# Optimization experiments

Hardware: AMD Instinct MI355X
Metric: run time of the kernel (lower is better)

The kernel has to match this reference:

```python
import jax, jax.numpy as jnp
import numpy as np

LN_EPS = 1e-5
SN_EPS = 1e-12


def _block(x, W, b, g, be):
    # Linear -> LayerNorm -> CELU, fused as one expression chain
    h = x @ W.T + b
    mu = jnp.mean(h, axis=-1, keepdims=True)
    var = jnp.mean(jnp.square(h - mu), axis=-1, keepdims=True)
    h = (h - mu) * jax.lax.rsqrt(var + LN_EPS) * g + be
    return jax.nn.celu(h)


def _spectral_norm_weight(W, u):
    # One power iteration (torch training-mode behavior), u/v detached.
    v = W.T @ u
    v = v / (jnp.linalg.norm(v) + SN_EPS)
    u2 = W @ v
    u2 = u2 / (jnp.linalg.norm(u2) + SN_EPS)
    sigma = u2 @ (W @ v)
    return W / sigma


def setup_inputs() -> dict:
    key = jax.random.key(0)
    ks = jax.random.split(key, 8)
    B, D = 131072, 512
    sizes = [512, 128, 32, 8]
    inp = {"x": jax.random.normal(ks[0], (B, D), dtype=jnp.float32)}
    fan_in = D
    for i, s in enumerate(sizes, start=1):
        scale = 1.0 / np.sqrt(fan_in)
        inp[f"W{i}"] = jax.random.normal(ks[i], (s, fan_in), dtype=jnp.float32) * scale
        inp[f"b{i}"] = jnp.zeros((s,), dtype=jnp.float32)
        inp[f"g{i}"] = jnp.ones((s,), dtype=jnp.float32)
        inp[f"be{i}"] = jnp.zeros((s,), dtype=jnp.float32)
        fan_in = s
    inp["Wh"] = jax.random.normal(ks[5], (1, 8), dtype=jnp.float32) * (1.0 / np.sqrt(8))
    inp["bh"] = jnp.zeros((1,), dtype=jnp.float32)
    inp["u"] = jax.random.normal(ks[6], (1,), dtype=jnp.float32)
    return inp


def reference(x, W1, b1, g1, be1, W2, b2, g2, be2, W3, b3, g3, be3,
              W4, b4, g4, be4, Wh, bh, u):
    h = _block(x, W1, b1, g1, be1)
    h = _block(h, W2, b2, g2, be2)
    h = _block(h, W3, b3, g3, be3)
    h = _block(h, W4, b4, g4, be4)          # hidden_output: [B, 8]
    Wsn = _spectral_norm_weight(Wh, u)
    return h @ Wsn.T + bh                   # [B, 1]
```

## Files before the change

### kernel.cpp

```cpp
#include <hip/hip_runtime.h>


typedef unsigned short u16;
typedef unsigned int   u32;
typedef __bf16  bf16x8 __attribute__((ext_vector_type(8)));
typedef float   f32x16 __attribute__((ext_vector_type(16)));

__device__ __forceinline__ u16 f2bf(float f) {
    u32 x = __builtin_bit_cast(u32, f);
    x += 0x7FFFu + ((x >> 16) & 1u);
    return (u16)(x >> 16);
}
__device__ __forceinline__ float bfval(u16 h) { return __builtin_bit_cast(float, (u32)h << 16); }
__device__ __forceinline__ u32 pack2(float a, float b) { return (u32)f2bf(a) | ((u32)f2bf(b) << 16); }
__device__ __forceinline__ float celu1(float x) { return x > 0.f ? x : __expf(x) - 1.f; }

#define W1F_OFF 0
#define W2F_OFF 262144
#define W3F_OFF 327680
#define W3LF_OFF 331776
#define NGROUPS 41984

__global__ void prep_weights(const float* __restrict__ W1, const float* __restrict__ W2,
                             const float* __restrict__ W3, u16* __restrict__ wsb) {
    const int g = blockIdx.x * 256 + threadIdx.x;
    if (g < 32768) {
        const int l = g & 63, t = (g >> 6) & 15, ksg = g >> 10;
        const int n = t * 32 + (l & 31);
        const int k0 = ksg * 16 + (l >> 5) * 8;
        u16* dst = wsb + W1F_OFF + g * 8;
        const float* src = W1 + n * 512 + k0;
#pragma unroll
        for (int e = 0; e < 8; ++e) dst[e] = f2bf(src[e]);
    } else if (g < 40960) {
        const int h = g - 32768;
        const int l = h & 63, t = (h >> 6) & 3, ksg = h >> 8;
        const int n = t * 32 + (l & 31);
        const int k0 = ksg * 16 + (l >> 5) * 8;
        u16* dst = wsb + W2F_OFF + h * 8;
        const float* src = W2 + n * 512 + k0;
#pragma unroll
        for (int e = 0; e < 8; ++e) dst[e] = f2bf(src[e]);
    } else if (g < 41472) {
        const int h = g - 40960;
        const int l = h & 63, ksg = h >> 6;
        const int n = l & 31;
        const int k0 = ksg * 16 + (l >> 5) * 8;
        u16* dst = wsb + W3F_OFF + h * 8;
        const float* src = W3 + n * 128 + k0;
#pragma unroll
        for (int e = 0; e < 8; ++e) dst[e] = f2bf(src[e]);
    } else {
        const int h = g - 41472;
        const int l = h & 63, ksg = h >> 6;
        const int n = l & 31;
        const int k0 = ksg * 16 + (l >> 5) * 8;
        u16* dst = wsb + W3LF_OFF + h * 8;
        const float* src = W3 + n * 128 + k0;
#pragma unroll
        for (int e = 0; e < 8; ++e) { float w = src[e]; dst[e] = f2bf(w - bfval(f2bf(w))); }
    }
}

#define PW4 0
#define PB4 256
#define PG4 264
#define PBE4 272
#define PWH 280
#define PBH 288
#define PU  289
#define NPAR 290

__global__ __launch_bounds__(512, 4) void fused_mlp(
    const float* __restrict__ x,
    const u16* __restrict__ W1b, const u16* __restrict__ W2b,
    const u16* __restrict__ W3b, const u16* __restrict__ W3Lb,
    const float* __restrict__ b1, const float* __restrict__ g1, const float* __restrict__ be1,
    const float* __restrict__ b2, const float* __restrict__ g2, const float* __restrict__ be2,
    const float* __restrict__ b3, const float* __restrict__ g3, const float* __restrict__ be3,
    const float* __restrict__ W4, const float* __restrict__ b4, const float* __restrict__ g4,
    const float* __restrict__ be4,
    const float* __restrict__ Wh, const float* __restrict__ bh, const float* __restrict__ uvec,
    float* __restrict__ out)
{
    __shared__ __align__(16) u16 sXH[32][520];
    __shared__ __align__(16) float sPS[32][8];
    __shared__ __align__(16) float sPQ[32][8];
    __shared__ __align__(8)  float2 sMR[32];
    __shared__ __align__(16) float sP[NPAR + 2];

    const int tid = threadIdx.x;
    const int wv = tid >> 6;
    const int lane = tid & 63;
    const int ln = lane & 31;
    const int lh = lane >> 5;
    const int row0 = blockIdx.x * 32;

    const float b1a = b1[wv * 64 + ln],  b1c = b1[wv * 64 + 32 + ln];
    const float g1a = g1[wv * 64 + ln],  g1c = g1[wv * 64 + 32 + ln];
    const float e1a = be1[wv * 64 + ln], e1c = be1[wv * 64 + 32 + ln];
    const int Nt2 = wv & 3;
    const float b2v = b2[Nt2 * 32 + ln], g2v = g2[Nt2 * 32 + ln], e2v = be2[Nt2 * 32 + ln];
    const float b3v = b3[ln], g3v = g3[ln], e3v = be3[ln];

    if (tid < NPAR) {
        float v;
        if      (tid < 256) v = W4[tid];
        else if (tid < 264) v = b4[tid - 256];
        else if (tid < 272) v = g4[tid - 264];
        else if (tid < 280) v = be4[tid - 272];
        else if (tid < 288) v = Wh[tid - 280];
        else if (tid == 288) v = bh[0];
        else                v = uvec[0];
        sP[tid] = v;
    }

    {
        const float4* xp = (const float4*)(x) + (long)blockIdx.x * 4096 + tid;
        float4 q[8];
#pragma unroll
        for (int j = 0; j < 8; ++j) q[j] = xp[j * 512];
        const int r0 = tid >> 7;
        const int c4 = (tid & 127) * 4;
#pragma unroll
        for (int j = 0; j < 8; ++j)
            *(uint2*)(&sXH[j * 4 + r0][c4]) =
                make_uint2(pack2(q[j].x, q[j].y), pack2(q[j].z, q[j].w));
    }
    __syncthreads();

    f32x16 acc[2] = {};
    {
        const u16* wq = W1b + (wv * 2) * 512 + lane * 8;
        bf16x8 Bf[4][2];
#pragma unroll
        for (int s = 0; s < 3; ++s) {
            Bf[s][0] = *(const bf16x8*)(wq + s * 8192);
            Bf[s][1] = *(const bf16x8*)(wq + s * 8192 + 512);
        }
#pragma unroll
        for (int ksg = 0; ksg < 32; ++ksg) {
            const int slot = ksg & 3;
            if (ksg + 3 < 32) {
                const int ps = (ksg + 3) & 3;
                const u16* np = wq + (ksg + 3) * 8192;
                Bf[ps][0] = *(const bf16x8*)(np);
                Bf[ps][1] = *(const bf16x8*)(np + 512);
            }
            bf16x8 a0 = *(const bf16x8*)(&sXH[ln][ksg * 16 + lh * 8]);
            acc[0] = __builtin_amdgcn_mfma_f32_32x32x16_bf16(a0, Bf[slot][0], acc[0], 0, 0, 0);
            acc[1] = __builtin_amdgcn_mfma_f32_32x32x16_bf16(a0, Bf[slot][1], acc[1], 0, 0, 0);
        }
    }

#pragma unroll
    for (int rg = 0; rg < 16; ++rg) {
        acc[0][rg] += b1a; acc[1][rg] += b1c;
    }
#pragma unroll
    for (int rg = 0; rg < 16; ++rg) {
        float s = acc[0][rg] + acc[1][rg];
        float q = acc[0][rg] * acc[0][rg] + acc[1][rg] * acc[1][rg];
#pragma unroll
        for (int m = 1; m < 32; m <<= 1) { s += __shfl_xor(s, m, 64); q += __shfl_xor(q, m, 64); }
        if (ln == 0) {
            const int row = (rg & 3) + 8 * (rg >> 2) + 4 * lh;
            sPS[row][wv] = s; sPQ[row][wv] = q;
        }
    }
    __syncthreads();
    if (tid < 32) {
        float s = 0.f, q = 0.f;
#pragma unroll
        for (int j = 0; j < 8; ++j) { s += sPS[tid][j]; q += sPQ[tid][j]; }
        const float mu = s * (1.f / 512.f);
        const float var = q * (1.f / 512.f) - mu * mu;
        sMR[tid] = make_float2(mu, rsqrtf(var + 1e-5f));
    }
    __syncthreads();
#pragma unroll
    for (int rg = 0; rg < 16; ++rg) {
        const int row = (rg & 3) + 8 * (rg >> 2) + 4 * lh;
        const float2 mr = sMR[row];
        const float h0 = (acc[0][rg] - mr.x) * mr.y * g1a + e1a;
        const float h1v = (acc[1][rg] - mr.x) * mr.y * g1c + e1c;
        sXH[row][wv * 64 + ln] = f2bf(celu1(h0));
        sXH[row][wv * 64 + 32 + ln] = f2bf(celu1(h1v));
    }
    __syncthreads();

    float v2[16];
    if (wv < 4) {
        const u16* w2q = W2b + Nt2 * 512 + lane * 8;
        bf16x8 W2f[4];
#pragma unroll
        for (int s = 0; s < 4; ++s) W2f[s] = *(const bf16x8*)(w2q + s * 2048);
        f32x16 a2 = {}, a2b = {};
        const u16* h1p = &sXH[ln][lh * 8];
#pragma unroll
        for (int ksg = 0; ksg < 32; ++ksg) {
            const int slot = ksg & 3;
            bf16x8 af = *(const bf16x8*)(h1p + ksg * 16);
            if (ksg & 1) a2b = __builtin_amdgcn_mfma_f32_32x32x16_bf16(af, W2f[slot], a2b, 0, 0, 0);
            else         a2  = __builtin_amdgcn_mfma_f32_32x32x16_bf16(af, W2f[slot], a2, 0, 0, 0);
            if (ksg + 4 < 32) W2f[slot] = *(const bf16x8*)(w2q + (ksg + 4) * 2048);
        }
#pragma unroll
        for (int rg = 0; rg < 16; ++rg) v2[rg] = a2[rg] + a2b[rg] + b2v;
#pragma unroll
        for (int rg = 0; rg < 16; ++rg) {
            float s = v2[rg], q = v2[rg] * v2[rg];
#pragma unroll
            for (int m = 1; m < 32; m <<= 1) { s += __shfl_xor(s, m, 64); q += __shfl_xor(q, m, 64); }
            if (ln == 0) {
                const int row = (rg & 3) + 8 * (rg >> 2) + 4 * lh;
                sPS[row][Nt2] = s; sPQ[row][Nt2] = q;
            }
        }
    }
    __syncthreads();
    if (tid < 32) {
        float s = sPS[tid][0] + sPS[tid][1] + sPS[tid][2] + sPS[tid][3];
        float q = sPQ[tid][0] + sPQ[tid][1] + sPQ[tid][2] + sPQ[tid][3];
        const float mu = s * (1.f / 128.f);
        const float var = q * (1.f / 128.f) - mu * mu;
        sMR[tid] = make_float2(mu, rsqrtf(var + 1e-5f));
    }
    __syncthreads();
    if (wv < 4) {
        const int col = Nt2 * 32 + ln;
#pragma unroll
        for (int rg = 0; rg < 16; ++rg) {
            const int row = (rg & 3) + 8 * (rg >> 2) + 4 * lh;
            const float2 mr = sMR[row];
            const float hn = (v2[rg] - mr.x) * mr.y * g2v + e2v;
            const float a = celu1(hn);
            const u16 hi = f2bf(a);
            sXH[row][col] = hi;
            sXH[row][128 + col] = f2bf(a - bfval(hi));
        }
    }
    __syncthreads();

    if (wv == 0) {
        f32x16 a3 = {};
        const u16* w3q  = W3b  + lane * 8;
        const u16* w3lq = W3Lb + lane * 8;
        const u16* h2p  = &sXH[ln][lh * 8];
        const u16* h2lp = &sXH[ln][128 + lh * 8];
#pragma unroll
        for (int ks = 0; ks < 8; ++ks) {
            bf16x8 fa_h = *(const bf16x8*)(h2p  + ks * 16);
            bf16x8 fa_l = *(const bf16x8*)(h2lp + ks * 16);
            bf16x8 fb_h = *(const bf16x8*)(w3q  + ks * 512);
            bf16x8 fb_l = *(const bf16x8*)(w3lq + ks * 512);
            a3 = __builtin_amdgcn_mfma_f32_32x32x16_bf16(fa_h, fb_h, a3, 0, 0, 0);
            a3 = __builtin_amdgcn_mfma_f32_32x32x16_bf16(fa_h, fb_l, a3, 0, 0, 0);
            a3 = __builtin_amdgcn_mfma_f32_32x32x16_bf16(fa_l, fb_h, a3, 0, 0, 0);
        }
#pragma unroll
        for (int rg = 0; rg < 16; ++rg) {
            const float v = a3[rg] + b3v;
            float s = v, q = v * v;
#pragma unroll
            for (int m = 1; m < 32; m <<= 1) { s += __shfl_xor(s, m, 64); q += __shfl_xor(q, m, 64); }
            const float mu = s * (1.f / 32.f);
            const float rs = rsqrtf(q * (1.f / 32.f) - mu * mu + 1e-5f);
            const int row = (rg & 3) + 8 * (rg >> 2) + 4 * lh;
            float* s3 = (float*)&sXH[row][0] + 128;
            s3[ln] = celu1((v - mu) * rs * g3v + e3v);
        }
    }
    __syncthreads();

    if (tid < 256) {
        const int r = tid & 31, o = tid >> 5;
        float h[32];
        const float4* hp = (const float4*)((const float*)&sXH[r][0] + 128);
#pragma unroll
        for (int j = 0; j < 8; ++j) {
            float4 tv = hp[j];
            h[j * 4 + 0] = tv.x; h[j * 4 + 1] = tv.y; h[j * 4 + 2] = tv.z; h[j * 4 + 3] = tv.w;
        }
        float a = sP[PB4 + o];
        const float* w4 = &sP[PW4 + o * 32];
#pragma unroll
        for (int k = 0; k < 32; ++k) a += h[k] * w4[k];
        sPS[r][o] = a;
    }
    __syncthreads();

    if (tid < 32) {
        float v[8];
        float s = 0.f, q = 0.f;
#pragma unroll
        for (int o = 0; o < 8; ++o) { v[o] = sPS[tid][o]; s += v[o]; q += v[o] * v[o]; }
        const float mu = s * 0.125f;
        const float var = q * 0.125f - mu * mu;
        const float rs = rsqrtf(var + 1e-5f);

        float wh[8];
        const float u0 = sP[PU];
        float nv = 0.f;
#pragma unroll
        for (int o = 0; o < 8; ++o) { wh[o] = sP[PWH + o]; float tt = wh[o] * u0; nv += tt * tt; }
        nv = sqrtf(nv);
        const float inv = 1.f / (nv + 1e-12f);
        float s2 = 0.f;
#pragma unroll
        for (int o = 0; o < 8; ++o) s2 += wh[o] * (wh[o] * u0 * inv);
        const float u2 = s2 / (fabsf(s2) + 1e-12f);
        const float sigma = u2 * s2;
        const float isg = 1.f / sigma;

        float y = sP[PBH];
#pragma unroll
        for (int o = 0; o < 8; ++o) {
            const float hn = (v[o] - mu) * rs * sP[PG4 + o] + sP[PBE4 + o];
            y += celu1(hn) * wh[o] * isg;
        }
        out[row0 + tid] = y;
    }
}

extern "C" void kernel_launch(void* const* d_in, const int* in_sizes, int n_in,
                              void* d_out, int out_size, void* d_ws, size_t ws_size,
                              hipStream_t stream) {
    const float* x   = (const float*)d_in[0];
    const float* W1  = (const float*)d_in[1];
    const float* b1  = (const float*)d_in[2];
    const float* g1  = (const float*)d_in[3];
    const float* be1 = (const float*)d_in[4];
    const float* W2  = (const float*)d_in[5];
    const float* b2  = (const float*)d_in[6];
    const float* g2  = (const float*)d_in[7];
    const float* be2 = (const float*)d_in[8];
    const float* W3  = (const float*)d_in[9];
    const float* b3  = (const float*)d_in[10];
    const float* g3  = (const float*)d_in[11];
    const float* be3 = (const float*)d_in[12];
    const float* W4  = (const float*)d_in[13];
    const float* b4  = (const float*)d_in[14];
    const float* g4  = (const float*)d_in[15];
    const float* be4 = (const float*)d_in[16];
    const float* Wh  = (const float*)d_in[17];
    const float* bh  = (const float*)d_in[18];
    const float* u   = (const float*)d_in[19];
    float* out = (float*)d_out;
    u16* wsb = (u16*)d_ws;

    prep_weights<<<dim3(NGROUPS / 256), dim3(256), 0, stream>>>(W1, W2, W3, wsb);

    const int rows = in_sizes[0] / 512;
    fused_mlp<<<dim3(rows / 32), dim3(512), 0, stream>>>(
        x, wsb + W1F_OFF, wsb + W2F_OFF, wsb + W3F_OFF, wsb + W3LF_OFF,
        b1, g1, be1, b2, g2, be2, b3, g3, be3,
        W4, b4, g4, be4, Wh, bh, u, out);
}
```

Measured before the change: 595.6 us.

## Halve block to 4 waves with 4 N-tiles each and drop tail barriers

Moves the fused MLP from 512-thread to 256-thread blocks. Each wave now computes four 32-column tiles of layer 1, and all four waves do useful work in layer 2 instead of leaving four idle. The layer-4/head stage is folded into wave 0 using an LDS waitcnt instead of block barriers, and s_setprio is raised around the MFMA loops. f2bf now uses the native bf16 conversion. In exchange, each wave holds more accumulator registers, and the W1 prefetch depth drops from three stages to two, which risks lower occupancy and more load latency exposed in layer 1.

Result: faster. 512.7 us (-13.9%).

```diff
diff --git a/kernel.cpp b/kernel.cpp
--- a/kernel.cpp
+++ b/kernel.cpp
@@ -7,9 +7,7 @@
 typedef float   f32x16 __attribute__((ext_vector_type(16)));
 
 __device__ __forceinline__ u16 f2bf(float f) {
-    u32 x = __builtin_bit_cast(u32, f);
-    x += 0x7FFFu + ((x >> 16) & 1u);
-    return (u16)(x >> 16);
+    return __builtin_bit_cast(u16, (__bf16)f);
 }
 __device__ __forceinline__ float bfval(u16 h) { return __builtin_bit_cast(float, (u32)h << 16); }
 __device__ __forceinline__ u32 pack2(float a, float b) { return (u32)f2bf(a) | ((u32)f2bf(b) << 16); }
@@ -71,7 +69,7 @@
 #define PU  289
 #define NPAR 290
 
-__global__ __launch_bounds__(512, 4) void fused_mlp(
+__global__ __launch_bounds__(256, 4) void fused_mlp(
     const float* __restrict__ x,
     const u16* __restrict__ W1b, const u16* __restrict__ W2b,
     const u16* __restrict__ W3b, const u16* __restrict__ W3Lb,
@@ -84,8 +82,8 @@
     float* __restrict__ out)
 {
     __shared__ __align__(16) u16 sXH[32][520];
-    __shared__ __align__(16) float sPS[32][8];
-    __shared__ __align__(16) float sPQ[32][8];
+    __shared__ __align__(16) float sPS[32][4];
+    __shared__ __align__(16) float sPQ[32][4];
     __shared__ __align__(8)  float2 sMR[32];
     __shared__ __align__(16) float sP[NPAR + 2];
 
@@ -96,71 +94,79 @@
     const int lh = lane >> 5;
     const int row0 = blockIdx.x * 32;
 
-    const float b1a = b1[wv * 64 + ln],  b1c = b1[wv * 64 + 32 + ln];
-    const float g1a = g1[wv * 64 + ln],  g1c = g1[wv * 64 + 32 + ln];
-    const float e1a = be1[wv * 64 + ln], e1c = be1[wv * 64 + 32 + ln];
-    const int Nt2 = wv & 3;
-    const float b2v = b2[Nt2 * 32 + ln], g2v = g2[Nt2 * 32 + ln], e2v = be2[Nt2 * 32 + ln];
+    float b1v[4], g1v[4], e1v[4];
+#pragma unroll
+    for (int nt = 0; nt < 4; ++nt) {
+        b1v[nt] = b1[wv * 128 + nt * 32 + ln];
+        g1v[nt] = g1[wv * 128 + nt * 32 + ln];
+        e1v[nt] = be1[wv * 128 + nt * 32 + ln];
+    }
+    const float b2v = b2[wv * 32 + ln], g2v = g2[wv * 32 + ln], e2v = be2[wv * 32 + ln];
     const float b3v = b3[ln], g3v = g3[ln], e3v = be3[ln];
 
-    if (tid < NPAR) {
+    for (int i = tid; i < NPAR; i += 256) {
         float v;
-        if      (tid < 256) v = W4[tid];
-        else if (tid < 264) v = b4[tid - 256];
-        else if (tid < 272) v = g4[tid - 264];
-        else if (tid < 280) v = be4[tid - 272];
-        else if (tid < 288) v = Wh[tid - 280];
-        else if (tid == 288) v = bh[0];
-        else                v = uvec[0];
-        sP[tid] = v;
+        if      (i < 256) v = W4[i];
+        else if (i < 264) v = b4[i - 256];
+        else if (i < 272) v = g4[i - 264];
+        else if (i < 280) v = be4[i - 272];
+        else if (i < 288) v = Wh[i - 280];
+        else if (i == 288) v = bh[0];
+        else               v = uvec[0];
+        sP[i] = v;
     }
 
     {
         const float4* xp = (const float4*)(x) + (long)blockIdx.x * 4096 + tid;
-        float4 q[8];
-#pragma unroll
-        for (int j = 0; j < 8; ++j) q[j] = xp[j * 512];
+        float4 q[16];
+#pragma unroll
+        for (int j = 0; j < 16; ++j) q[j] = xp[j * 256];
         const int r0 = tid >> 7;
         const int c4 = (tid & 127) * 4;
 #pragma unroll
-        for (int j = 0; j < 8; ++j)
-            *(uint2*)(&sXH[j * 4 + r0][c4]) =
+        for (int j = 0; j < 16; ++j)
+            *(uint2*)(&sXH[j * 2 + r0][c4]) =
                 make_uint2(pack2(q[j].x, q[j].y), pack2(q[j].z, q[j].w));
     }
     __syncthreads();
 
-    f32x16 acc[2] = {};
-    {
-        const u16* wq = W1b + (wv * 2) * 512 + lane * 8;
-        bf16x8 Bf[4][2];
-#pragma unroll
-        for (int s = 0; s < 3; ++s) {
-            Bf[s][0] = *(const bf16x8*)(wq + s * 8192);
-            Bf[s][1] = *(const bf16x8*)(wq + s * 8192 + 512);
-        }
+    f32x16 acc[4] = {};
+    {
+        const u16* wq = W1b + (wv * 4) * 512 + lane * 8;
+        bf16x8 Bf[2][4];
+#pragma unroll
+        for (int s = 0; s < 2; ++s)
+#pragma unroll
+            for (int nt = 0; nt < 4; ++nt)
+                Bf[s][nt] = *(const bf16x8*)(wq + s * 8192 + nt * 512);
+        __builtin_amdgcn_s_setprio(1);
 #pragma unroll
         for (int ksg = 0; ksg < 32; ++ksg) {
-            const int slot = ksg & 3;
-            if (ksg + 3 < 32) {
-                const int ps = (ksg + 3) & 3;
-                const u16* np = wq + (ksg + 3) * 8192;
-                Bf[ps][0] = *(const bf16x8*)(np);
-                Bf[ps][1] = *(const bf16x8*)(np + 512);
-            }
+            const int slot = ksg & 1;
             bf16x8 a0 = *(const bf16x8*)(&sXH[ln][ksg * 16 + lh * 8]);
             acc[0] = __builtin_amdgcn_mfma_f32_32x32x16_bf16(a0, Bf[slot][0], acc[0], 0, 0, 0);
             acc[1] = __builtin_amdgcn_mfma_f32_32x32x16_bf16(a0, Bf[slot][1], acc[1], 0, 0, 0);
-        }
-    }
-
+            acc[2] = __builtin_amdgcn_mfma_f32_32x32x16_bf16(a0, Bf[slot][2], acc[2], 0, 0, 0);
+            acc[3] = __builtin_amdgcn_mfma_f32_32x32x16_bf16(a0, Bf[slot][3], acc[3], 0, 0, 0);
+            if (ksg + 2 < 32) {
+                const u16* np = wq + (ksg + 2) * 8192;
+#pragma unroll
+                for (int nt = 0; nt < 4; ++nt)
+                    Bf[slot][nt] = *(const bf16x8*)(np + nt * 512);
+            }
+        }
+        __builtin_amdgcn_s_setprio(0);
+    }
+
+#pragma unroll
+    for (int nt = 0; nt < 4; ++nt)
+#pragma unroll
+        for (int rg = 0; rg < 16; ++rg) acc[nt][rg] += b1v[nt];
 #pragma unroll
     for (int rg = 0; rg < 16; ++rg) {
-        acc[0][rg] += b1a; acc[1][rg] += b1c;
-    }
-#pragma unroll
-    for (int rg = 0; rg < 16; ++rg) {
-        float s = acc[0][rg] + acc[1][rg];
-        float q = acc[0][rg] * acc[0][rg] + acc[1][rg] * acc[1][rg];
+        float s = acc[0][rg] + acc[1][rg] + acc[2][rg] + acc[3][rg];
+        float q = acc[0][rg] * acc[0][rg] + acc[1][rg] * acc[1][rg]
+                + acc[2][rg] * acc[2][rg] + acc[3][rg] * acc[3][rg];
 #pragma unroll
         for (int m = 1; m < 32; m <<= 1) { s += __shfl_xor(s, m, 64); q += __shfl_xor(q, m, 64); }
         if (ln == 0) {
@@ -170,9 +176,8 @@
     }
     __syncthreads();
     if (tid < 32) {
-        float s = 0.f, q = 0.f;
-#pragma unroll
-        for (int j = 0; j < 8; ++j) { s += sPS[tid][j]; q += sPQ[tid][j]; }
+        const float s = sPS[tid][0] + sPS[tid][1] + sPS[tid][2] + sPS[tid][3];
+        const float q = sPQ[tid][0] + sPQ[tid][1] + sPQ[tid][2] + sPQ[tid][3];
         const float mu = s * (1.f / 512.f);
         const float var = q * (1.f / 512.f) - mu * mu;
         sMR[tid] = make_float2(mu, rsqrtf(var + 1e-5f));
@@ -182,21 +187,23 @@
     for (int rg = 0; rg < 16; ++rg) {
         const int row = (rg & 3) + 8 * (rg >> 2) + 4 * lh;
         const float2 mr = sMR[row];
-        const float h0 = (acc[0][rg] - mr.x) * mr.y * g1a + e1a;
-        const float h1v = (acc[1][rg] - mr.x) * mr.y * g1c + e1c;
-        sXH[row][wv * 64 + ln] = f2bf(celu1(h0));
-        sXH[row][wv * 64 + 32 + ln] = f2bf(celu1(h1v));
+#pragma unroll
+        for (int nt = 0; nt < 4; ++nt) {
+            const float h0 = (acc[nt][rg] - mr.x) * mr.y * g1v[nt] + e1v[nt];
+            sXH[row][wv * 128 + nt * 32 + ln] = f2bf(celu1(h0));
+        }
     }
     __syncthreads();
 
     float v2[16];
-    if (wv < 4) {
-        const u16* w2q = W2b + Nt2 * 512 + lane * 8;
+    {
+        const u16* w2q = W2b + wv * 512 + lane * 8;
         bf16x8 W2f[4];
 #pragma unroll
         for (int s = 0; s < 4; ++s) W2f[s] = *(const bf16x8*)(w2q + s * 2048);
         f32x16 a2 = {}, a2b = {};
         const u16* h1p = &sXH[ln][lh * 8];
+        __builtin_amdgcn_s_setprio(1);
 #pragma unroll
         for (int ksg = 0; ksg < 32; ++ksg) {
             const int slot = ksg & 3;
@@ -205,6 +212,7 @@
             else         a2  = __builtin_amdgcn_mfma_f32_32x32x16_bf16(af, W2f[slot], a2, 0, 0, 0);
             if (ksg + 4 < 32) W2f[slot] = *(const bf16x8*)(w2q + (ksg + 4) * 2048);
         }
+        __builtin_amdgcn_s_setprio(0);
 #pragma unroll
         for (int rg = 0; rg < 16; ++rg) v2[rg] = a2[rg] + a2b[rg] + b2v;
 #pragma unroll
@@ -214,21 +222,21 @@
             for (int m = 1; m < 32; m <<= 1) { s += __shfl_xor(s, m, 64); q += __shfl_xor(q, m, 64); }
             if (ln == 0) {
                 const int row = (rg & 3) + 8 * (rg >> 2) + 4 * lh;
-                sPS[row][Nt2] = s; sPQ[row][Nt2] = q;
+                sPS[row][wv] = s; sPQ[row][wv] = q;
             }
         }
     }
     __syncthreads();
     if (tid < 32) {
-        float s = sPS[tid][0] + sPS[tid][1] + sPS[tid][2] + sPS[tid][3];
-        float q = sPQ[tid][0] + sPQ[tid][1] + sPQ[tid][2] + sPQ[tid][3];
+        const float s = sPS[tid][0] + sPS[tid][1] + sPS[tid][2] + sPS[tid][3];
+        const float q = sPQ[tid][0] + sPQ[tid][1] + sPQ[tid][2] + sPQ[tid][3];
         const float mu = s * (1.f / 128.f);
         const float var = q * (1.f / 128.f) - mu * mu;
         sMR[tid] = make_float2(mu, rsqrtf(var + 1e-5f));
     }
     __syncthreads();
-    if (wv < 4) {
-        const int col = Nt2 * 32 + ln;
+    {
+        const int col = wv * 32 + ln;
 #pragma unroll
         for (int rg = 0; rg < 16; ++rg) {
             const int row = (rg & 3) + 8 * (rg >> 2) + 4 * lh;
@@ -242,7 +250,9 @@
     }
     __syncthreads();
 
-    if (wv == 0) {
+    if (wv != 0) return;
+
+    {
         f32x16 a3 = {};
         const u16* w3q  = W3b  + lane * 8;
         const u16* w3lq = W3Lb + lane * 8;
@@ -271,10 +281,10 @@
             s3[ln] = celu1((v - mu) * rs * g3v + e3v);
         }
     }
-    __syncthreads();
-
-    if (tid < 256) {
-        const int r = tid & 31, o = tid >> 5;
+    __asm__ volatile("s_waitcnt lgkmcnt(0)" ::: "memory");
+
+    if (lane < 32) {
+        const int r = lane;
         float h[32];
         const float4* hp = (const float4*)((const float*)&sXH[r][0] + 128);
 #pragma unroll
@@ -282,19 +292,16 @@
             float4 tv = hp[j];
             h[j * 4 + 0] = tv.x; h[j * 4 + 1] = tv.y; h[j * 4 + 2] = tv.z; h[j * 4 + 3] = tv.w;
         }
-        float a = sP[PB4 + o];
-        const float* w4 = &sP[PW4 + o * 32];
-#pragma unroll
-        for (int k = 0; k < 32; ++k) a += h[k] * w4[k];
-        sPS[r][o] = a;
-    }
-    __syncthreads();
-
-    if (tid < 32) {
         float v[8];
         float s = 0.f, q = 0.f;
 #pragma unroll
-        for (int o = 0; o < 8; ++o) { v[o] = sPS[tid][o]; s += v[o]; q += v[o] * v[o]; }
+        for (int o = 0; o < 8; ++o) {
+            float a = sP[PB4 + o];
+            const float* w4 = &sP[PW4 + o * 32];
+#pragma unroll
+            for (int k = 0; k < 32; ++k) a += h[k] * w4[k];
+            v[o] = a; s += a; q += a * a;
+        }
         const float mu = s * 0.125f;
         const float var = q * 0.125f - mu * mu;
         const float rs = rsqrtf(var + 1e-5f);
@@ -319,7 +326,7 @@
             const float hn = (v[o] - mu) * rs * sP[PG4 + o] + sP[PBE4 + o];
             y += celu1(hn) * wh[o] * isg;
         }
-        out[row0 + tid] = y;
+        out[row0 + r] = y;
     }
 }
 
@@ -352,7 +359,7 @@
     prep_weights<<<dim3(NGROUPS / 256), dim3(256), 0, stream>>>(W1, W2, W3, wsb);
 
     const int rows = in_sizes[0] / 512;
-    fused_mlp<<<dim3(rows / 32), dim3(512), 0, stream>>>(
+    fused_mlp<<<dim3(rows / 32), dim3(256), 0, stream>>>(
         x, wsb + W1F_OFF, wsb + W2F_OFF, wsb + W3F_OFF, wsb + W3LF_OFF,
         b1, g1, be1, b2, g2, be2, b3, g3, be3,
         W4, b4, g4, be4, Wh, bh, u, out);
```
